# Kernel optimization log

Hardware: AMD Instinct MI355X
Metric: run time of the kernel (lower is better)

Reference implementation:

```python
import jax, jax.numpy as jnp
import numpy as np

N = 204800            # total nodes
B = 128               # graphs in batch
PER = N // B          # 1600 nodes per graph
THREAD_STRIDE = 10    # every 10th node is a 'thread' node
DEG = 160             # in-degree of each thread node
EDGE_DIM = 65         # edge_attr feature dim; message dim = EDGE_DIM-1 = 64
MSG_DIM = EDGE_DIM - 1
FFN_DIMS = (128, 64)
NUM_CLASSES = 2

THREAD_PATTERN = jnp.array([0.0, 0.0, 0.0, 0.0, 1.0], dtype=jnp.float32)
NONTHREAD_PATTERN = jnp.array([1.0, 0.0, 0.0, 0.0, 0.0], dtype=jnp.float32)


def setup_inputs() -> dict:
    key = jax.random.key(0)
    ks = jax.random.split(key, 6)

    idx = jnp.arange(N)
    thread_mask = (idx % THREAD_STRIDE) == 0                      # [N]
    x = jnp.where(thread_mask[:, None], THREAD_PATTERN, NONTHREAD_PATTERN)  # [N,5]

    thread_idx = idx[::THREAD_STRIDE]                             # [N/10]
    tgt = jnp.repeat(thread_idx, DEG)                             # [E] every thread node has DEG in-edges
    E = tgt.shape[0]
    src = jax.random.randint(ks[0], (E,), 0, N)
    edge_index = jnp.stack([src, tgt]).astype(jnp.int32)          # [2,E]

    edge_attr = jax.random.uniform(ks[1], (E, EDGE_DIM), dtype=jnp.float32)

    batch = jnp.repeat(jnp.arange(B, dtype=jnp.int32), PER)       # [N] contiguous graphs
    ptr = (jnp.arange(B + 1, dtype=jnp.int32) * PER)              # [B+1]

    # learned params
    weights = jnp.ones((MSG_DIM,), dtype=jnp.float32)             # Weighted_Sum_Aggregator init ones_
    W1 = jax.random.normal(ks[2], (MSG_DIM, FFN_DIMS[0]), dtype=jnp.float32) * 0.05
    b1 = jnp.zeros((FFN_DIMS[0],), dtype=jnp.float32)
    W2 = jax.random.normal(ks[3], (FFN_DIMS[0], FFN_DIMS[1]), dtype=jnp.float32) * 0.05
    b2 = jnp.zeros((FFN_DIMS[1],), dtype=jnp.float32)
    W3 = jax.random.normal(ks[4], (FFN_DIMS[1], NUM_CLASSES), dtype=jnp.float32) * 0.05
    b3 = jnp.zeros((NUM_CLASSES,), dtype=jnp.float32)

    return {"x": x, "edge_index": edge_index, "edge_attr": edge_attr,
            "batch": batch, "ptr": ptr, "weights": weights,
            "W1": W1, "b1": b1, "W2": W2, "b2": b2, "W3": W3, "b3": b3}


def reference(x, edge_index, edge_attr, batch, ptr, weights, W1, b1, W2, b2, W3, b3):
    # --- message: slice off last edge_attr column ---
    msg = edge_attr[:, :-1]                                       # [E, MSG_DIM]
    tgt = edge_index[1]                                           # [E] aggregation index

    # --- scatter-sum aggregation into target nodes, then elementwise weight ---
    per_node = jax.ops.segment_sum(msg, tgt, num_segments=N)      # [N, MSG_DIM]
    weighted = per_node * weights[None, :]                        # Weighted_Sum_Aggregator

    # --- keep only 'thread' nodes (x[:, :5] == [0,0,0,0,1]) ---
    thread_mask = jnp.all(x[:, :5] == THREAD_PATTERN.astype(x.dtype), axis=1)  # [N]

    # --- global max pool over thread nodes per graph (batch id == bucketize(idx, ptr)-1) ---
    vals = jnp.where(thread_mask[:, None], weighted, -jnp.inf)    # non-thread rows excluded
    pooled = jax.ops.segment_max(vals, batch, num_segments=B)     # [B, MSG_DIM]

    # --- FFN (dropout = identity in eval), final Softmax ---
    h = jax.nn.relu(pooled @ W1 + b1)
    h = jax.nn.relu(h @ W2 + b2)
    return jax.nn.softmax(h @ W3 + b3, axis=1)                    # [B, NUM_CLASSES]
```

## Files before the change

kernel.cpp:

```cpp
#include <hip/hip_runtime.h>
#include <math.h>

#define DEG      160
#define EDGE_DIM 65
#define MSGD     64
#define NODE_FLOATS (DEG * EDGE_DIM)
#define STRIPES  (NODE_FLOATS / 260)

typedef float f32x4 __attribute__((ext_vector_type(4)));

__global__ __launch_bounds__(256) void gnn_segsum_kernel(
    const float* __restrict__ x,
    const int*   __restrict__ tgt,
    const float* __restrict__ edge_attr,
    const float* __restrict__ weights,
    float*       __restrict__ sums,
    int NT)
{
    __shared__ float bins[4][72];

    int w    = threadIdx.x >> 6;
    int lane = threadIdx.x & 63;
    int node_task = blockIdx.x * 4 + w;
    bool active = node_task < NT;

    bins[w][lane] = 0.0f;
    if (lane == 0) bins[w][64] = 0.0f;
    __syncthreads();

    bool mask = false;
    if (active) {
        int node = tgt[(size_t)node_task * DEG];
        const float* xr = x + (size_t)node * 5;
        mask = (xr[0] == 0.0f) && (xr[1] == 0.0f) && (xr[2] == 0.0f) &&
               (xr[3] == 0.0f) && (xr[4] == 1.0f);
    }

    if (active) {
        const float* base = edge_attr + (size_t)node_task * NODE_FLOATS;
        const f32x4* p    = reinterpret_cast<const f32x4*>(base) + lane;

        float a0 = 0.0f, a1 = 0.0f, a2 = 0.0f, a3 = 0.0f;
        #pragma unroll 8
        for (int s = 0; s < STRIPES; ++s) {
            f32x4 v = __builtin_nontemporal_load(&p[(size_t)s * 65]);
            a0 += v.x; a1 += v.y; a2 += v.z; a3 += v.w;
        }

        int c0 = (4 * lane)     % 65;
        int c1 = (4 * lane + 1) % 65;
        int c2 = (4 * lane + 2) % 65;
        int c3 = (4 * lane + 3) % 65;
        if (c0 != 64) atomicAdd(&bins[w][c0], a0);
        if (c1 != 64) atomicAdd(&bins[w][c1], a1);
        if (c2 != 64) atomicAdd(&bins[w][c2], a2);
        if (c3 != 64) atomicAdd(&bins[w][c3], a3);

        if (lane < STRIPES) {
            const f32x4* tp = reinterpret_cast<const f32x4*>(base + (size_t)lane * 260 + 256);
            f32x4 t4 = __builtin_nontemporal_load(tp);
            atomicAdd(&bins[w][61], t4.x);
            atomicAdd(&bins[w][62], t4.y);
            atomicAdd(&bins[w][63], t4.z);
        }
    }
    __syncthreads();

    if (active) {
        float v = mask ? bins[w][lane] * weights[lane] : -INFINITY;
        sums[(size_t)node_task * MSGD + lane] = v;
    }
}

__global__ __launch_bounds__(256) void gnn_pool_ffn_kernel(
    const float* __restrict__ sums,
    const float* __restrict__ W1, const float* __restrict__ b1,
    const float* __restrict__ W2, const float* __restrict__ b2,
    const float* __restrict__ W3, const float* __restrict__ b3,
    float*       __restrict__ out,
    int TPB)
{
    __shared__ float part[4][64];
    __shared__ float pooled_s[MSGD];
    __shared__ float h1_s[128];

    int b    = blockIdx.x;
    int tid  = threadIdx.x;
    int w    = tid >> 6;
    int lane = tid & 63;

    const float* srow = sums + (size_t)b * TPB * MSGD;

    float m0 = -INFINITY, m1 = -INFINITY, m2 = -INFINITY, m3 = -INFINITY;
    for (int t = w * 4; t < TPB; t += 16) {
        m0 = fmaxf(m0, srow[(size_t)(t + 0) * MSGD + lane]);
        if (t + 1 < TPB) m1 = fmaxf(m1, srow[(size_t)(t + 1) * MSGD + lane]);
        if (t + 2 < TPB) m2 = fmaxf(m2, srow[(size_t)(t + 2) * MSGD + lane]);
        if (t + 3 < TPB) m3 = fmaxf(m3, srow[(size_t)(t + 3) * MSGD + lane]);
    }
    part[w][lane] = fmaxf(fmaxf(m0, m1), fmaxf(m2, m3));
    __syncthreads();

    if (tid < 64) {
        pooled_s[lane] = fmaxf(fmaxf(part[0][lane], part[1][lane]),
                               fmaxf(part[2][lane], part[3][lane]));
    }
    __syncthreads();

    if (tid < 128) {
        float a = b1[tid];
        #pragma unroll 8
        for (int d = 0; d < MSGD; ++d) {
            a += pooled_s[d] * W1[d * 128 + tid];
        }
        h1_s[tid] = fmaxf(a, 0.0f);
    }
    __syncthreads();

    if (tid < 64) {
        float a2 = b2[tid];
        #pragma unroll 8
        for (int j = 0; j < 128; ++j) {
            a2 += h1_s[j] * W2[j * 64 + tid];
        }
        float h2 = fmaxf(a2, 0.0f);

        float l0 = h2 * W3[tid * 2 + 0];
        float l1 = h2 * W3[tid * 2 + 1];
        #pragma unroll
        for (int off = 32; off > 0; off >>= 1) {
            l0 += __shfl_down(l0, off);
            l1 += __shfl_down(l1, off);
        }

        if (lane == 0) {
            l0 += b3[0];
            l1 += b3[1];
            float mx = fmaxf(l0, l1);
            float e0 = __expf(l0 - mx);
            float e1 = __expf(l1 - mx);
            float inv = 1.0f / (e0 + e1);
            out[b * 2 + 0] = e0 * inv;
            out[b * 2 + 1] = e1 * inv;
        }
    }
}

extern "C" void kernel_launch(void* const* d_in, const int* in_sizes, int n_in,
                              void* d_out, int out_size, void* d_ws, size_t ws_size,
                              hipStream_t stream)
{
    const float* x   = (const float*)d_in[0];
    const int*   ei  = (const int*)  d_in[1];
    const float* ea  = (const float*)d_in[2];
    const float* w   = (const float*)d_in[5];
    const float* W1  = (const float*)d_in[6];
    const float* b1  = (const float*)d_in[7];
    const float* W2  = (const float*)d_in[8];
    const float* b2  = (const float*)d_in[9];
    const float* W3  = (const float*)d_in[10];
    const float* b3  = (const float*)d_in[11];

    int E  = in_sizes[1] / 2;
    int NT = E / DEG;
    int Bn = out_size / 2;
    int TPB = NT / Bn;
    const int* tgt = ei + E;

    float* sums = (float*)d_ws;

    int blocks1 = (NT + 3) / 4;
    gnn_segsum_kernel<<<blocks1, 256, 0, stream>>>(x, tgt, ea, w, sums, NT);
    gnn_pool_ffn_kernel<<<Bn, 256, 0, stream>>>(sums, W1, b1, W2, b2, W3, b3,
                                                (float*)d_out, TPB);
}
```

Measured before the change: 163.4 us.

## Fuse per-graph max pooling into segsum kernel via global float atomic max

The segment-sum kernel now reduces its four node results per block and applies an atomic float max straight into a per-graph pooled buffer. This removes the intermediate per-node sums array and the pooling pass that read it back. An init kernel sets the buffer to -inf, and the FFN kernel shrinks to 128 threads that read the pooled vector directly. It adds one small launch and global atomics, and it assumes each block's four nodes belong to the same graph, which holds because TPB is a multiple of 4.

Result: faster. 155.4 us (-4.9%).

```diff
diff --git a/kernel.cpp b/kernel.cpp
--- a/kernel.cpp
+++ b/kernel.cpp
@@ -9,15 +9,30 @@
 
 typedef float f32x4 __attribute__((ext_vector_type(4)));
 
+__device__ inline void atomicMaxFloat(float* addr, float val) {
+    if (val >= 0.0f) {
+        atomicMax((int*)addr, __float_as_int(val));
+    } else {
+        atomicMin((unsigned int*)addr, __float_as_uint(val));
+    }
+}
+
+__global__ void gnn_init_kernel(float* __restrict__ gmax, int n)
+{
+    int i = blockIdx.x * blockDim.x + threadIdx.x;
+    if (i < n) gmax[i] = -INFINITY;
+}
+
 __global__ __launch_bounds__(256) void gnn_segsum_kernel(
     const float* __restrict__ x,
     const int*   __restrict__ tgt,
     const float* __restrict__ edge_attr,
     const float* __restrict__ weights,
-    float*       __restrict__ sums,
-    int NT)
+    float*       __restrict__ gmax,
+    int NT, int TPB)
 {
     __shared__ float bins[4][72];
+    __shared__ int   wmask[4];
 
     int w    = threadIdx.x >> 6;
     int lane = threadIdx.x & 63;
@@ -25,7 +40,7 @@
     bool active = node_task < NT;
 
     bins[w][lane] = 0.0f;
-    if (lane == 0) bins[w][64] = 0.0f;
+    if (lane == 0) { bins[w][64] = 0.0f; wmask[w] = 0; }
     __syncthreads();
 
     bool mask = false;
@@ -63,51 +78,42 @@
             atomicAdd(&bins[w][62], t4.y);
             atomicAdd(&bins[w][63], t4.z);
         }
+        if (lane == 0 && mask) wmask[w] = 1;
     }
     __syncthreads();
 
-    if (active) {
-        float v = mask ? bins[w][lane] * weights[lane] : -INFINITY;
-        sums[(size_t)node_task * MSGD + lane] = v;
+    if (threadIdx.x < 64) {
+        float wl = weights[lane];
+        float vmax = -INFINITY;
+        #pragma unroll
+        for (int ww = 0; ww < 4; ++ww) {
+            if (wmask[ww]) vmax = fmaxf(vmax, bins[ww][lane] * wl);
+        }
+        int node_base = blockIdx.x * 4;
+        if (node_base < NT && vmax != -INFINITY) {
+            int batch = node_base / TPB;
+            atomicMaxFloat(&gmax[(size_t)batch * MSGD + lane], vmax);
+        }
     }
 }
 
-__global__ __launch_bounds__(256) void gnn_pool_ffn_kernel(
-    const float* __restrict__ sums,
+__global__ __launch_bounds__(128) void gnn_ffn_kernel(
+    const float* __restrict__ gmax,
     const float* __restrict__ W1, const float* __restrict__ b1,
     const float* __restrict__ W2, const float* __restrict__ b2,
     const float* __restrict__ W3, const float* __restrict__ b3,
-    float*       __restrict__ out,
-    int TPB)
+    float*       __restrict__ out)
 {
-    __shared__ float part[4][64];
     __shared__ float pooled_s[MSGD];
     __shared__ float h1_s[128];
 
-    int b    = blockIdx.x;
-    int tid  = threadIdx.x;
-    int w    = tid >> 6;
-    int lane = tid & 63;
+    int b   = blockIdx.x;
+    int tid = threadIdx.x;
 
-    const float* srow = sums + (size_t)b * TPB * MSGD;
-
-    float m0 = -INFINITY, m1 = -INFINITY, m2 = -INFINITY, m3 = -INFINITY;
-    for (int t = w * 4; t < TPB; t += 16) {
-        m0 = fmaxf(m0, srow[(size_t)(t + 0) * MSGD + lane]);
-        if (t + 1 < TPB) m1 = fmaxf(m1, srow[(size_t)(t + 1) * MSGD + lane]);
-        if (t + 2 < TPB) m2 = fmaxf(m2, srow[(size_t)(t + 2) * MSGD + lane]);
-        if (t + 3 < TPB) m3 = fmaxf(m3, srow[(size_t)(t + 3) * MSGD + lane]);
-    }
-    part[w][lane] = fmaxf(fmaxf(m0, m1), fmaxf(m2, m3));
+    if (tid < 64) pooled_s[tid] = gmax[(size_t)b * MSGD + tid];
     __syncthreads();
 
-    if (tid < 64) {
-        pooled_s[lane] = fmaxf(fmaxf(part[0][lane], part[1][lane]),
-                               fmaxf(part[2][lane], part[3][lane]));
-    }
-    __syncthreads();
-
-    if (tid < 128) {
+    {
         float a = b1[tid];
         #pragma unroll 8
         for (int d = 0; d < MSGD; ++d) {
@@ -133,7 +139,7 @@
             l1 += __shfl_down(l1, off);
         }
 
-        if (lane == 0) {
+        if (tid == 0) {
             l0 += b3[0];
             l1 += b3[1];
             float mx = fmaxf(l0, l1);
@@ -167,10 +173,14 @@
     int TPB = NT / Bn;
     const int* tgt = ei + E;
 
-    float* sums = (float*)d_ws;
+    float* gmax = (float*)d_ws;
+
+    int ng = Bn * MSGD;
+    gnn_init_kernel<<<(ng + 255) / 256, 256, 0, stream>>>(gmax, ng);
 
     int blocks1 = (NT + 3) / 4;
-    gnn_segsum_kernel<<<blocks1, 256, 0, stream>>>(x, tgt, ea, w, sums, NT);
-    gnn_pool_ffn_kernel<<<Bn, 256, 0, stream>>>(sums, W1, b1, W2, b2, W3, b3,
-                                                (float*)d_out, TPB);
+    gnn_segsum_kernel<<<blocks1, 256, 0, stream>>>(x, tgt, ea, w, gmax, NT, TPB);
+
+    gnn_ffn_kernel<<<Bn, 128, 0, stream>>>(gmax, W1, b1, W2, b2, W3, b3,
+                                           (float*)d_out);
 }
```
